# Optimization experiments

Hardware: AMD Instinct MI355X
Metric: run time of the kernel (lower is better)

## Reference

```python
import jax, jax.numpy as jnp
import numpy as np

T, N, F, H = 64, 20000, 8, 32
E = 320000
NEG_SLOPE = 0.01  # torch.nn.LeakyReLU default


def setup_inputs() -> dict:
    key = jax.random.key(0)
    ks = jax.random.split(key, 16)
    g = lambda k, shape, fan_in: jax.random.normal(k, shape, jnp.float32) * (1.0 / np.sqrt(fan_in))
    return {
        "x": jax.random.normal(ks[0], (T, N, F), jnp.float32),
        "edge_index": jax.random.randint(ks[1], (2, E), 0, N, jnp.int64),
        "edge_weight": jax.random.uniform(ks[2], (E,), jnp.float32),
        "h": jnp.zeros((N, H), jnp.float32),
        # GConvGRU(K=1): each ChebConv reduces to a dense Linear (only T_0 = X term)
        "Wxz": g(ks[3], (F, H), F), "bxz": jnp.zeros((H,), jnp.float32),
        "Whz": g(ks[4], (H, H), H), "bhz": jnp.zeros((H,), jnp.float32),
        "Wxr": g(ks[5], (F, H), F), "bxr": jnp.zeros((H,), jnp.float32),
        "Whr": g(ks[6], (H, H), H), "bhr": jnp.zeros((H,), jnp.float32),
        "Wxh": g(ks[7], (F, H), F), "bxh": jnp.zeros((H,), jnp.float32),
        "Whh": g(ks[8], (H, H), H), "bhh": jnp.zeros((H,), jnp.float32),
        "W1": g(ks[9], (H, 1), H), "b1": jnp.zeros((1,), jnp.float32),
        "W2": g(ks[10], (N, 1), N), "b2": jnp.zeros((1,), jnp.float32),
    }


def reference(x, edge_index, edge_weight, h,
              Wxz, bxz, Whz, bhz, Wxr, bxr, Whr, bhr, Wxh, bxh, Whh, bhh,
              W1, b1, W2, b2):
    # GConvGRU with Chebyshev order K=1: each ChebConv is out = X @ W + b
    # (edge_index / edge_weight only participate for K >= 2, faithful to source).
    def gru_step(hc, xt):  # hc: [N,H], xt: [N,F]
        z = jax.nn.sigmoid(xt @ Wxz + bxz + hc @ Whz + bhz)
        r = jax.nn.sigmoid(xt @ Wxr + bxr + hc @ Whr + bhr)
        h_tilde = jnp.tanh(xt @ Wxh + bxh + (hc * r) @ Whh + bhh)
        hn = z * hc + (1.0 - z) * h_tilde
        return hn, hn

    h_fin, h_tensor = jax.lax.scan(gru_step, h, x)  # h_tensor: [T,N,H]
    a = jax.nn.leaky_relu(h_tensor, NEG_SLOPE)       # LeakyReLU(h_tensor)
    a = jax.nn.leaky_relu(a @ W1 + b1, NEG_SLOPE)    # linear1 -> [T,N,1], then LeakyReLU
    a = a[..., 0]                                    # squeeze -> [T,N]
    out = (a @ W2 + b2)[..., 0]                      # linear2 -> [T,1] -> squeeze -> [T]
    return (out, h_fin)
```

## Files before the change

### kernel.cpp

```cpp
#include <hip/hip_runtime.h>
#include <hip/hip_bf16.h>

#define T_STEPS 64
#define N_NODES 20000
#define F_IN    8
#define H_DIM   32
#define NEG_SLOPE 0.01f
#define WS_STRIDE 32
#define LOG2E 1.44269504f

typedef __attribute__((ext_vector_type(8))) short bf16x8;
typedef __attribute__((ext_vector_type(4))) float f32x4;

#define MFMA(a, b, c) __builtin_amdgcn_mfma_f32_16x16x32_bf16((a), (b), (c), 0, 0, 0)

__device__ __forceinline__ unsigned short f2bf(float f) {
    unsigned u = __float_as_uint(f);
    u += 0x7FFFu + ((u >> 16) & 1u);
    return (unsigned short)(u >> 16);
}
__device__ __forceinline__ float bf2f(unsigned short s) {
    return __uint_as_float(((unsigned)s) << 16);
}
__device__ __forceinline__ void split_pack8_rne(const float* v, bf16x8& hi, bf16x8& lo) {
    union { unsigned u[4]; bf16x8 v8; } H, L;
#pragma unroll
    for (int p = 0; p < 4; ++p) {
        float a = v[2*p], b = v[2*p+1];
        unsigned short ha = f2bf(a), hb = f2bf(b);
        unsigned short la = f2bf(a - bf2f(ha)), lb = f2bf(b - bf2f(hb));
        H.u[p] = (unsigned)ha | ((unsigned)hb << 16);
        L.u[p] = (unsigned)la | ((unsigned)lb << 16);
    }
    hi = H.v8; lo = L.v8;
}

__device__ __forceinline__ unsigned cvtpk(float a, float b) {
    union { __hip_bfloat162 h; unsigned u; } U;
    U.h = __float22bfloat162_rn(float2{a, b});
    return U.u;
}


__device__ __forceinline__ void load_wfragW(const float* __restrict__ W, int c, int q,
                                            int Rout, int Rown, int Roth, float scale,
                                            bf16x8& hi, bf16x8& lo) {
    float v[8];
#pragma unroll
    for (int j = 0; j < 8; ++j) {
        int dim = (j < 4) ? (Rown + 4*q + j) : (Roth + 4*q + (j - 4));
        v[j] = W[dim * H_DIM + (Rout + c)] * scale;
    }
    split_pack8_rne(v, hi, lo);
}

__device__ __forceinline__ bf16x8 load_xwfragW(const float* __restrict__ Wx,
                                               const float* __restrict__ bx,
                                               const float* __restrict__ bh,
                                               int c, int q, int Rout, float scale) {
    union { unsigned short s[8]; bf16x8 v8; } U;
#pragma unroll
    for (int j = 0; j < 8; ++j) U.s[j] = 0;
    if (q == 0) {
#pragma unroll
        for (int j = 0; j < 8; ++j) U.s[j] = f2bf(Wx[j * H_DIM + Rout + c] * scale);
    } else if (q == 1) {
#pragma unroll
        for (int j = 0; j < 8; ++j) {
            float w0 = Wx[j * H_DIM + Rout + c] * scale;
            unsigned short h = f2bf(w0);
            U.s[j] = f2bf(w0 - bf2f(h));
        }
    } else if (q == 3) {
        float b = (bx[Rout + c] + bh[Rout + c]) * scale;
        unsigned short h = f2bf(b);
        U.s[0] = h;
        U.s[1] = f2bf(b - bf2f(h));
    }
    return U.v8;
}

__device__ __forceinline__ bf16x8 build_xbfrag2(const float* v, int q) {
    union { unsigned u[4]; bf16x8 v8; } U;
#pragma unroll
    for (int p = 0; p < 4; ++p) {
        unsigned val = cvtpk(v[2*p], v[2*p+1]);
        if (q == 2) val = 0u;
        if (q == 3) val = (p == 0) ? 0x3F803F80u : 0u;
        U.u[p] = val;
    }
    return U.v8;
}

__device__ __forceinline__ float sigmoid2_f(float xp) {
    return __builtin_amdgcn_rcpf(1.0f + __builtin_amdgcn_exp2f(-xp));
}
__device__ __forceinline__ float tanh2_f(float yp) {
    return 1.0f - 2.0f * __builtin_amdgcn_rcpf(1.0f + __builtin_amdgcn_exp2f(yp));
}
__device__ __forceinline__ float leaky_f(float x) {
    return fmaxf(x, NEG_SLOPE * x);
}

__global__ void final_kernel(const float* __restrict__ ws, const float* __restrict__ b2,
                             float* __restrict__ out) {
    int t = threadIdx.x;
    if (t < T_STEPS) out[t] = ws[t * WS_STRIDE] + b2[0];
}

__global__ __launch_bounds__(128, 3) void rgcn_mfma_kernel(
    const float* __restrict__ x,
    const float* __restrict__ h0,
    const float* __restrict__ Wxz, const float* __restrict__ bxz,
    const float* __restrict__ Whz, const float* __restrict__ bhz,
    const float* __restrict__ Wxr, const float* __restrict__ bxr,
    const float* __restrict__ Whr, const float* __restrict__ bhr,
    const float* __restrict__ Wxh, const float* __restrict__ bxh,
    const float* __restrict__ Whh, const float* __restrict__ bhh,
    const float* __restrict__ W1,  const float* __restrict__ b1,
    const float* __restrict__ W2,
    float* __restrict__ ws,
    float* __restrict__ out)
{
    const int tid  = threadIdx.x;
    const int w    = tid >> 6;
    const int l    = tid & 63;
    const int c    = l & 15;
    const int q    = l >> 4;
    const int base = blockIdx.x * 16;
    const int node = base + c;
    const int Rown = 16 * w;
    const int Roth = 16 - Rown;

    __shared__ __align__(16) float hxbuf[2][2][4][16][4];
    __shared__ unsigned short pbuf16[T_STEPS][130];

    bf16x8 WHrOh, WHrOl, WHrTh, WHrTl, WHzh, WHzl, WHhh, WHhl;
    load_wfragW(Whr, c, q, Rown, Rown, Roth, LOG2E,        WHrOh, WHrOl);
    load_wfragW(Whr, c, q, Roth, Rown, Roth, LOG2E,        WHrTh, WHrTl);
    load_wfragW(Whz, c, q, Rown, Rown, Roth, LOG2E,        WHzh,  WHzl);
    load_wfragW(Whh, c, q, Rown, Rown, Roth, 2.0f * LOG2E, WHhh,  WHhl);
    bf16x8 WXrO = load_xwfragW(Wxr, bxr, bhr, c, q, Rown, LOG2E);
    bf16x8 WXrT = load_xwfragW(Wxr, bxr, bhr, c, q, Roth, LOG2E);
    bf16x8 WXz  = load_xwfragW(Wxz, bxz, bhz, c, q, Rown, LOG2E);
    bf16x8 WXh  = load_xwfragW(Wxh, bxh, bhh, c, q, Rown, 2.0f * LOG2E);

    float w1v[4];
#pragma unroll
    for (int i = 0; i < 4; ++i) w1v[i] = W1[Rown + 4*q + i];
    const float b1s = b1[0];
    const float w2l = W2[node];

    float hv8[8];
    unsigned own01, own23;
    {
        float4 h4 = ((const float4*)(h0 + (size_t)node * H_DIM + Rown))[q];
        hv8[0] = h4.x; hv8[1] = h4.y; hv8[2] = h4.z; hv8[3] = h4.w;
        *(float4*)&hxbuf[0][w][q][c][0] = h4;
        own01 = cvtpk(hv8[0], hv8[1]);
        own23 = cvtpk(hv8[2], hv8[3]);
    }

    const f32x4 zero4 = {0.0f, 0.0f, 0.0f, 0.0f};

    f32x4 axrO, axrT, axz, axh;
    {
        const float4* xp = (const float4*)(x + (size_t)node * F_IN);
        float4 x0 = xp[0], x1 = xp[1];
        float xv[8] = {x0.x, x0.y, x0.z, x0.w, x1.x, x1.y, x1.z, x1.w};
        bf16x8 fx0 = build_xbfrag2(xv, q);
        axrO = MFMA(WXrO, fx0, zero4);
        axrT = MFMA(WXrT, fx0, zero4);
        axz  = MFMA(WXz,  fx0, zero4);
        axh  = MFMA(WXh,  fx0, zero4);
    }
    float4 cx0, cx1;
    {
        const float4* xp = (const float4*)(x + (size_t)(N_NODES * F_IN)
                                             + (size_t)node * F_IN);
        cx0 = xp[0]; cx1 = xp[1];
    }

    __syncthreads();

#pragma unroll 1
    for (int t = 0; t < T_STEPS; ++t) {
        const int rp = t & 1;

        int tt = (t + 2 < T_STEPS) ? (t + 2) : (T_STEPS - 1);
        const float4* xp = (const float4*)(x + (size_t)tt * (N_NODES * F_IN)
                                             + (size_t)node * F_IN);
        float4 nx0 = xp[0], nx1 = xp[1];

        float4 oh = *(const float4*)&hxbuf[rp][1 - w][q][c][0];
        hv8[4] = oh.x; hv8[5] = oh.y; hv8[6] = oh.z; hv8[7] = oh.w;

        union { unsigned u[4]; bf16x8 v8; } FH;
        FH.u[0] = own01; FH.u[1] = own23;
        FH.u[2] = cvtpk(oh.x, oh.y);
        FH.u[3] = cvtpk(oh.z, oh.w);
        bf16x8 fhh = FH.v8;

        f32x4 arOB = MFMA(WHrOl, fhh, zero4);
        f32x4 arOA = MFMA(WHrOh, fhh, axrO);
        f32x4 arTB = MFMA(WHrTl, fhh, zero4);
        f32x4 arTA = MFMA(WHrTh, fhh, axrT);
        f32x4 az   = MFMA(WHzh,  fhh, axz);
        az         = MFMA(WHzl,  fhh, az);

        f32x4 arO = arOA + arOB;
        f32x4 arT = arTA + arTB;

        float rh8[8];
#pragma unroll
        for (int i = 0; i < 4; ++i) {
            rh8[i]     = sigmoid2_f(arO[i]) * hv8[i];
            rh8[4 + i] = sigmoid2_f(arT[i]) * hv8[4 + i];
        }
        union { unsigned u[4]; bf16x8 v8; } FR;
        FR.u[0] = cvtpk(rh8[0], rh8[1]);
        FR.u[1] = cvtpk(rh8[2], rh8[3]);
        FR.u[2] = cvtpk(rh8[4], rh8[5]);
        FR.u[3] = cvtpk(rh8[6], rh8[7]);
        bf16x8 frh = FR.v8;

        f32x4 ahB = MFMA(WHhl, frh, zero4);
        f32x4 ahA = MFMA(WHhh, frh, axh);

        float nxv[8] = {cx0.x, cx0.y, cx0.z, cx0.w, cx1.x, cx1.y, cx1.z, cx1.w};
        bf16x8 fxn = build_xbfrag2(nxv, q);

        f32x4 ah = ahA + ahB;

        float pnew = 0.0f;
#pragma unroll
        for (int i = 0; i < 4; ++i) {
            float zz = sigmoid2_f(az[i]);
            float th = tanh2_f(ah[i]);
            float hn = th + zz * (hv8[i] - th);
            hv8[i] = hn;
            pnew = fmaf(leaky_f(hn), w1v[i], pnew);
        }
        pbuf16[t][tid] = f2bf(pnew);

        own01 = cvtpk(hv8[0], hv8[1]);
        own23 = cvtpk(hv8[2], hv8[3]);
        *(float4*)&hxbuf[1 - rp][w][q][c][0] =
            (float4){hv8[0], hv8[1], hv8[2], hv8[3]};

        axrO = MFMA(WXrO, fxn, zero4);
        axrT = MFMA(WXrT, fxn, zero4);
        axz  = MFMA(WXz,  fxn, zero4);
        axh  = MFMA(WXh,  fxn, zero4);

        cx0 = nx0; cx1 = nx1;

        __syncthreads();
    }

#pragma unroll
    for (int rep = 0; rep < 8; ++rep) {
        int t = w * 32 + rep * 4 + q;
        float s = 0.0f;
#pragma unroll
        for (int g = 0; g < 8; ++g) s += bf2f(pbuf16[t][g * 16 + c]);
        float a2 = leaky_f(s + b1s) * w2l;
        a2 += __shfl_xor(a2, 1); a2 += __shfl_xor(a2, 2);
        a2 += __shfl_xor(a2, 4); a2 += __shfl_xor(a2, 8);
        if (c == 0) atomicAdd(&ws[t * WS_STRIDE], a2);
    }

    *(float4*)(out + T_STEPS + (size_t)node * H_DIM + Rown + 4*q) =
        (float4){hv8[0], hv8[1], hv8[2], hv8[3]};
}

extern "C" void kernel_launch(void* const* d_in, const int* in_sizes, int n_in,
                              void* d_out, int out_size, void* d_ws, size_t ws_size,
                              hipStream_t stream) {
    const float* x    = (const float*)d_in[0];
    const float* h0   = (const float*)d_in[3];
    const float* Wxz  = (const float*)d_in[4];
    const float* bxz  = (const float*)d_in[5];
    const float* Whz  = (const float*)d_in[6];
    const float* bhz  = (const float*)d_in[7];
    const float* Wxr  = (const float*)d_in[8];
    const float* bxr  = (const float*)d_in[9];
    const float* Whr  = (const float*)d_in[10];
    const float* bhr  = (const float*)d_in[11];
    const float* Wxh  = (const float*)d_in[12];
    const float* bxh  = (const float*)d_in[13];
    const float* Whh  = (const float*)d_in[14];
    const float* bhh  = (const float*)d_in[15];
    const float* W1   = (const float*)d_in[16];
    const float* b1   = (const float*)d_in[17];
    const float* W2   = (const float*)d_in[18];
    const float* b2   = (const float*)d_in[19];
    float* out = (float*)d_out;
    float* ws  = (float*)d_ws;

    const int grid = N_NODES / 16;
    rgcn_mfma_kernel<<<grid, 128, 0, stream>>>(
        x, h0, Wxz, bxz, Whz, bhz, Wxr, bxr, Whr, bhr,
        Wxh, bxh, Whh, bhh, W1, b1, W2, ws, out);

    final_kernel<<<1, 64, 0, stream>>>(ws, b2, out);
}
```

Measured before the change: 193.5 us.

## Exchange r*h via shared memory instead of redundantly computing the other wave's reset gate

Each wave now computes the reset gate only for its own 16 hidden units and writes r*h to a shared buffer. A second barrier per step lets it read the partner wave's half for the candidate MFMA. This removes two MFMAs per step for the other half's reset gate, plus one input MFMA and its weight registers. In exchange each timestep gets an extra __syncthreads on the serial recurrence path. The next-step input MFMAs are moved into the barrier gap, and the bf16 rounding of pnew now uses cvtpk.

```diff
diff --git a/kernel.cpp b/kernel.cpp
--- a/kernel.cpp
+++ b/kernel.cpp
@@ -133,15 +133,14 @@
     const int Roth = 16 - Rown;
 
     __shared__ __align__(16) float hxbuf[2][2][4][16][4];
+    __shared__ __align__(16) float rhbuf[2][4][16][4];
     __shared__ unsigned short pbuf16[T_STEPS][130];
 
-    bf16x8 WHrOh, WHrOl, WHrTh, WHrTl, WHzh, WHzl, WHhh, WHhl;
+    bf16x8 WHrOh, WHrOl, WHzh, WHzl, WHhh, WHhl;
     load_wfragW(Whr, c, q, Rown, Rown, Roth, LOG2E,        WHrOh, WHrOl);
-    load_wfragW(Whr, c, q, Roth, Rown, Roth, LOG2E,        WHrTh, WHrTl);
     load_wfragW(Whz, c, q, Rown, Rown, Roth, LOG2E,        WHzh,  WHzl);
     load_wfragW(Whh, c, q, Rown, Rown, Roth, 2.0f * LOG2E, WHhh,  WHhl);
     bf16x8 WXrO = load_xwfragW(Wxr, bxr, bhr, c, q, Rown, LOG2E);
-    bf16x8 WXrT = load_xwfragW(Wxr, bxr, bhr, c, q, Roth, LOG2E);
     bf16x8 WXz  = load_xwfragW(Wxz, bxz, bhz, c, q, Rown, LOG2E);
     bf16x8 WXh  = load_xwfragW(Wxh, bxh, bhh, c, q, Rown, 2.0f * LOG2E);
 
@@ -151,26 +150,25 @@
     const float b1s = b1[0];
     const float w2l = W2[node];
 
-    float hv8[8];
+    float hv[4];
     unsigned own01, own23;
     {
         float4 h4 = ((const float4*)(h0 + (size_t)node * H_DIM + Rown))[q];
-        hv8[0] = h4.x; hv8[1] = h4.y; hv8[2] = h4.z; hv8[3] = h4.w;
+        hv[0] = h4.x; hv[1] = h4.y; hv[2] = h4.z; hv[3] = h4.w;
         *(float4*)&hxbuf[0][w][q][c][0] = h4;
-        own01 = cvtpk(hv8[0], hv8[1]);
-        own23 = cvtpk(hv8[2], hv8[3]);
+        own01 = cvtpk(hv[0], hv[1]);
+        own23 = cvtpk(hv[2], hv[3]);
     }
 
     const f32x4 zero4 = {0.0f, 0.0f, 0.0f, 0.0f};
 
-    f32x4 axrO, axrT, axz, axh;
+    f32x4 axrO, axz, axh;
     {
         const float4* xp = (const float4*)(x + (size_t)node * F_IN);
         float4 x0 = xp[0], x1 = xp[1];
         float xv[8] = {x0.x, x0.y, x0.z, x0.w, x1.x, x1.y, x1.z, x1.w};
         bf16x8 fx0 = build_xbfrag2(xv, q);
         axrO = MFMA(WXrO, fx0, zero4);
-        axrT = MFMA(WXrT, fx0, zero4);
         axz  = MFMA(WXz,  fx0, zero4);
         axh  = MFMA(WXh,  fx0, zero4);
     }
@@ -193,7 +191,6 @@
         float4 nx0 = xp[0], nx1 = xp[1];
 
         float4 oh = *(const float4*)&hxbuf[rp][1 - w][q][c][0];
-        hv8[4] = oh.x; hv8[5] = oh.y; hv8[6] = oh.z; hv8[7] = oh.w;
 
         union { unsigned u[4]; bf16x8 v8; } FH;
         FH.u[0] = own01; FH.u[1] = own23;
@@ -201,58 +198,57 @@
         FH.u[3] = cvtpk(oh.z, oh.w);
         bf16x8 fhh = FH.v8;
 
-        f32x4 arOB = MFMA(WHrOl, fhh, zero4);
-        f32x4 arOA = MFMA(WHrOh, fhh, axrO);
-        f32x4 arTB = MFMA(WHrTl, fhh, zero4);
-        f32x4 arTA = MFMA(WHrTh, fhh, axrT);
-        f32x4 az   = MFMA(WHzh,  fhh, axz);
-        az         = MFMA(WHzl,  fhh, az);
-
-        f32x4 arO = arOA + arOB;
-        f32x4 arT = arTA + arTB;
-
-        float rh8[8];
-#pragma unroll
-        for (int i = 0; i < 4; ++i) {
-            rh8[i]     = sigmoid2_f(arO[i]) * hv8[i];
-            rh8[4 + i] = sigmoid2_f(arT[i]) * hv8[4 + i];
-        }
+        f32x4 arB = MFMA(WHrOl, fhh, zero4);
+        f32x4 arA = MFMA(WHrOh, fhh, axrO);
+        f32x4 az  = MFMA(WHzh,  fhh, axz);
+        az        = MFMA(WHzl,  fhh, az);
+        f32x4 arO = arA + arB;
+
+        float rh4[4];
+#pragma unroll
+        for (int i = 0; i < 4; ++i) rh4[i] = sigmoid2_f(arO[i]) * hv[i];
+        *(float4*)&rhbuf[w][q][c][0] = (float4){rh4[0], rh4[1], rh4[2], rh4[3]};
+
+        float nxv[8] = {cx0.x, cx0.y, cx0.z, cx0.w, cx1.x, cx1.y, cx1.z, cx1.w};
+        bf16x8 fxn = build_xbfrag2(nxv, q);
+        float zv[4];
+#pragma unroll
+        for (int i = 0; i < 4; ++i) zv[i] = sigmoid2_f(az[i]);
+
+        __syncthreads();
+
+        f32x4 nxrO = MFMA(WXrO, fxn, zero4);
+        f32x4 nxz  = MFMA(WXz,  fxn, zero4);
+        f32x4 nxh  = MFMA(WXh,  fxn, zero4);
+
+        float4 orh = *(const float4*)&rhbuf[1 - w][q][c][0];
+
         union { unsigned u[4]; bf16x8 v8; } FR;
-        FR.u[0] = cvtpk(rh8[0], rh8[1]);
-        FR.u[1] = cvtpk(rh8[2], rh8[3]);
-        FR.u[2] = cvtpk(rh8[4], rh8[5]);
-        FR.u[3] = cvtpk(rh8[6], rh8[7]);
+        FR.u[0] = cvtpk(rh4[0], rh4[1]);
+        FR.u[1] = cvtpk(rh4[2], rh4[3]);
+        FR.u[2] = cvtpk(orh.x, orh.y);
+        FR.u[3] = cvtpk(orh.z, orh.w);
         bf16x8 frh = FR.v8;
 
         f32x4 ahB = MFMA(WHhl, frh, zero4);
         f32x4 ahA = MFMA(WHhh, frh, axh);
-
-        float nxv[8] = {cx0.x, cx0.y, cx0.z, cx0.w, cx1.x, cx1.y, cx1.z, cx1.w};
-        bf16x8 fxn = build_xbfrag2(nxv, q);
-
-        f32x4 ah = ahA + ahB;
+        f32x4 ah  = ahA + ahB;
 
         float pnew = 0.0f;
 #pragma unroll
         for (int i = 0; i < 4; ++i) {
-            float zz = sigmoid2_f(az[i]);
             float th = tanh2_f(ah[i]);
-            float hn = th + zz * (hv8[i] - th);
-            hv8[i] = hn;
+            float hn = th + zv[i] * (hv[i] - th);
+            hv[i] = hn;
             pnew = fmaf(leaky_f(hn), w1v[i], pnew);
         }
-        pbuf16[t][tid] = f2bf(pnew);
-
-        own01 = cvtpk(hv8[0], hv8[1]);
-        own23 = cvtpk(hv8[2], hv8[3]);
-        *(float4*)&hxbuf[1 - rp][w][q][c][0] =
-            (float4){hv8[0], hv8[1], hv8[2], hv8[3]};
-
-        axrO = MFMA(WXrO, fxn, zero4);
-        axrT = MFMA(WXrT, fxn, zero4);
-        axz  = MFMA(WXz,  fxn, zero4);
-        axh  = MFMA(WXh,  fxn, zero4);
-
+        pbuf16[t][tid] = (unsigned short)cvtpk(pnew, pnew);
+
+        own01 = cvtpk(hv[0], hv[1]);
+        own23 = cvtpk(hv[2], hv[3]);
+        *(float4*)&hxbuf[1 - rp][w][q][c][0] = (float4){hv[0], hv[1], hv[2], hv[3]};
+
+        axrO = nxrO; axz = nxz; axh = nxh;
         cx0 = nx0; cx1 = nx1;
 
         __syncthreads();
@@ -271,7 +267,7 @@
     }
 
     *(float4*)(out + T_STEPS + (size_t)node * H_DIM + Rown + 4*q) =
-        (float4){hv8[0], hv8[1], hv8[2], hv8[3]};
+        (float4){hv[0], hv[1], hv[2], hv[3]};
 }
 
 extern "C" void kernel_launch(void* const* d_in, const int* in_sizes, int n_in,
```

Result: faster. 182.5 us (-5.7%).
